# Performance work log

Measured on AMD Instinct MI355X. Metric: run time of the kernel, lower is better.

## Reference

```python
import jax, jax.numpy as jnp
import numpy as np

STRIDE = 1  # module init arg


def setup_inputs() -> dict:
    key = jax.random.key(0)
    k1, k2 = jax.random.split(key)
    x = jax.random.normal(k1, (16, 32, 256, 256), dtype=jnp.float32)
    kernel = jax.random.normal(k2, (32, 5, 5), dtype=jnp.float32) * 0.1
    return {"input": x, "kernel": kernel}


def _maxmin_conv(x, kernel, stride=STRIDE):
    # Max-min semifield convolution:
    #   out[b,oc,i,j] = max_{c,dy,dx} min(x_pad[b,c,i*s+dy,j*s+dx], k[oc,dy,dx])
    # Since min(., k) is monotone in x, the max over in-channels commutes:
    #   max_{c} min(x_c, k) == min(max_c x_c, k)
    # so we reduce channels once up front (same math, far less memory).
    K = kernel.shape[-1]
    p = K - 1
    top = p // 2
    bot = p - top  # calculate_padding(): left=top=floor(p/2), right=bottom=p-top
    xmax = jnp.max(x, axis=1)  # [B, H, W]
    xp = jnp.pad(xmax, ((0, 0), (top, bot), (top, bot)), constant_values=-np.inf)
    B, Hp, Wp = xp.shape
    Ho = (Hp - K) // stride + 1
    Wo = (Wp - K) // stride + 1
    OC = kernel.shape[0]
    acc = jnp.full((B, OC, Ho, Wo), -np.inf, dtype=x.dtype)
    for dy in range(K):  # fixed small K*K loop over kernel taps
        for dx in range(K):
            patch = xp[:, dy:dy + stride * Ho:stride, dx:dx + stride * Wo:stride]  # [B,Ho,Wo]
            cand = jnp.minimum(patch[:, None, :, :], kernel[None, :, dy, dx, None, None])
            acc = jnp.maximum(acc, cand)
    return acc


def reference(input, kernel):
    return _maxmin_conv(input, kernel)
```

## Files before the change

### kernel.cpp

```cpp
#include <hip/hip_runtime.h>
#include <math.h>


#define BATCH 16
#define CH    32
#define OCH   32
#define HH    256
#define WW    256
#define HWSZ  (HH * WW)
#define TW    32
#define TH    32
#define LW    40
#define LH    36
#define NWG   (BATCH * (WW / TW) * (HH / TH))

__device__ __forceinline__ float vmax3(float a, float b, float c) {
    float d;
    asm("v_max3_f32 %0, %1, %2, %3" : "=v"(d) : "v"(a), "v"(b), "v"(c));
    return d;
}

__global__ __launch_bounds__(256, 3) void fused_maxmin_kernel(const float* __restrict__ x,
                                                              const float* __restrict__ kk,
                                                              float* __restrict__ out) {
    __shared__ float xmt[LH][LW];
    __shared__ float lkf[OCH * 25];

    int tid = threadIdx.x;
    int bid = blockIdx.x;
    int swz = (bid & 7) * (NWG >> 3) + (bid >> 3);
    int b   = swz >> 6;
    int ty  = (swz >> 3) & 7;
    int tx  = swz & 7;

    for (int i = tid; i < OCH * 25; i += 256) lkf[i] = kk[i];

    const float NI = -INFINITY;
    int x4base = tx * (TW / 4) - 1;
    int ybase  = ty * TH - 2;
    const float4* xb = (const float4*)(x + (size_t)b * CH * HWSZ);

    for (int p = tid; p < (LW / 4) * LH; p += 256) {
        int pc = p % (LW / 4);
        int pr = p / (LW / 4);
        int c4 = x4base + pc;
        int rw = ybase + pr;
        bool valid = (c4 >= 0) && (c4 < WW / 4) && (rw >= 0) && (rw < HH);
        int c4c = c4 < 0 ? 0 : (c4 > WW / 4 - 1 ? WW / 4 - 1 : c4);
        int rwc = rw < 0 ? 0 : (rw > HH - 1 ? HH - 1 : rw);
        const float4* src = xb + (size_t)rwc * (WW / 4) + c4c;
        float4 m = src[0];
#pragma unroll
        for (int c = 1; c < CH; ++c) {
            float4 v = src[(size_t)c * (HWSZ / 4)];
            m.x = fmaxf(m.x, v.x);
            m.y = fmaxf(m.y, v.y);
            m.z = fmaxf(m.z, v.z);
            m.w = fmaxf(m.w, v.w);
        }
        if (!valid) { m.x = NI; m.y = NI; m.z = NI; m.w = NI; }
        *(float4*)&xmt[pr][pc * 4] = m;
    }
    __syncthreads();

    int xg = tid & 7;
    int yg = (tid >> 3) & 3;
    int og = tid >> 5;
    int orow0 = yg * 8;

    const float* wbase = &xmt[0][4 * xg];

    for (int oi = 0; oi < 4; ++oi) {
        int o = og * 4 + oi;
        float kr[25];
#pragma unroll
        for (int i = 0; i < 25; ++i) kr[i] = lkf[o * 25 + i];

        float w[5][12];
#pragma unroll
        for (int r = 0; r < 4; ++r)
#pragma unroll
            for (int q = 0; q < 3; ++q)
                *(float4*)&w[r][4 * q] = *(const float4*)(wbase + (orow0 + r) * LW + 4 * q);

        float* op = out + (size_t)(b * OCH + o) * HWSZ
                  + (size_t)(ty * TH + orow0) * WW + tx * TW + 4 * xg;

#pragma unroll
        for (int r = 0; r < 8; ++r) {
            int wl = (r + 4) % 5;
#pragma unroll
            for (int q = 0; q < 3; ++q)
                *(float4*)&w[wl][4 * q] = *(const float4*)(wbase + (orow0 + r + 4) * LW + 4 * q);

            float a[4];
#pragma unroll
            for (int j = 0; j < 4; ++j) {
                float m[25];
#pragma unroll
                for (int dy = 0; dy < 5; ++dy) {
                    int wr = (r + dy) % 5;
#pragma unroll
                    for (int dx = 0; dx < 5; ++dx)
                        m[dy * 5 + dx] = fminf(w[wr][j + dx + 2], kr[dy * 5 + dx]);
                }
                float t0 = vmax3(m[0],  m[1],  m[2]);
                float t1 = vmax3(m[3],  m[4],  m[5]);
                float t2 = vmax3(m[6],  m[7],  m[8]);
                float t3 = vmax3(m[9],  m[10], m[11]);
                float t4 = vmax3(m[12], m[13], m[14]);
                float t5 = vmax3(m[15], m[16], m[17]);
                float t6 = vmax3(m[18], m[19], m[20]);
                float t7 = vmax3(m[21], m[22], m[23]);
                float u0 = vmax3(t0, t1, t2);
                float u1 = vmax3(t3, t4, t5);
                float u2 = vmax3(t6, t7, m[24]);
                a[j] = vmax3(u0, u1, u2);
            }
            *(float4*)(op + (size_t)r * WW) = make_float4(a[0], a[1], a[2], a[3]);
        }
    }
}

extern "C" void kernel_launch(void* const* d_in, const int* in_sizes, int n_in,
                              void* d_out, int out_size, void* d_ws, size_t ws_size,
                              hipStream_t stream) {
    const float* x  = (const float*)d_in[0];
    const float* kk = (const float*)d_in[1];
    float* out      = (float*)d_out;
    fused_maxmin_kernel<<<NWG, 256, 0, stream>>>(x, kk, out);
}
```

Measured before the change: 66.10 us.

## Remap compute threads to 2x8 output tiles with register-resident window across channels

Changes the thread-to-output mapping so each thread computes a 2-row by 8-column patch for 8 output channels, loading its 6x12 input window from LDS once into registers and reusing it across all channels. Kernel weights are now read directly from global memory with wave-uniform indexing (scalar loads) instead of staged in LDS. LDS row pitch is padded to 44 floats and occupancy hint raised to 4 blocks per SIMD. Trades fewer LDS reads for higher register pressure and more global output writes per thread.

```diff
diff --git a/kernel.cpp b/kernel.cpp
--- a/kernel.cpp
+++ b/kernel.cpp
@@ -10,7 +10,7 @@
 #define HWSZ  (HH * WW)
 #define TW    32
 #define TH    32
-#define LW    40
+#define LW    44
 #define LH    36
 #define NWG   (BATCH * (WW / TW) * (HH / TH))
 
@@ -20,12 +20,10 @@
     return d;
 }
 
-__global__ __launch_bounds__(256, 3) void fused_maxmin_kernel(const float* __restrict__ x,
+__global__ __launch_bounds__(256, 4) void fused_maxmin_kernel(const float* __restrict__ x,
                                                               const float* __restrict__ kk,
                                                               float* __restrict__ out) {
     __shared__ float xmt[LH][LW];
-    __shared__ float lkf[OCH * 25];
-
     int tid = threadIdx.x;
     int bid = blockIdx.x;
     int swz = (bid & 7) * (NWG >> 3) + (bid >> 3);
@@ -33,22 +31,20 @@
     int ty  = (swz >> 3) & 7;
     int tx  = swz & 7;
 
-    for (int i = tid; i < OCH * 25; i += 256) lkf[i] = kk[i];
-
     const float NI = -INFINITY;
-    int x4base = tx * (TW / 4) - 1;
-    int ybase  = ty * TH - 2;
+    int x4base = tx * 8 - 1;
+    int ybase  = ty * 32 - 2;
     const float4* xb = (const float4*)(x + (size_t)b * CH * HWSZ);
 
-    for (int p = tid; p < (LW / 4) * LH; p += 256) {
-        int pc = p % (LW / 4);
-        int pr = p / (LW / 4);
+    for (int p = tid; p < 10 * LH; p += 256) {
+        int pc = p % 10;
+        int pr = p / 10;
         int c4 = x4base + pc;
-        int rw = ybase + pr;
-        bool valid = (c4 >= 0) && (c4 < WW / 4) && (rw >= 0) && (rw < HH);
+        int rg = ybase + pr;
+        bool valid = (c4 >= 0) && (c4 < WW / 4) && (rg >= 0) && (rg < HH);
         int c4c = c4 < 0 ? 0 : (c4 > WW / 4 - 1 ? WW / 4 - 1 : c4);
-        int rwc = rw < 0 ? 0 : (rw > HH - 1 ? HH - 1 : rw);
-        const float4* src = xb + (size_t)rwc * (WW / 4) + c4c;
+        int rgc = rg < 0 ? 0 : (rg > HH - 1 ? HH - 1 : rg);
+        const float4* src = xb + (size_t)rgc * (WW / 4) + c4c;
         float4 m = src[0];
 #pragma unroll
         for (int c = 1; c < CH; ++c) {
@@ -63,47 +59,45 @@
     }
     __syncthreads();
 
-    int xg = tid & 7;
-    int yg = (tid >> 3) & 3;
-    int og = tid >> 5;
-    int orow0 = yg * 8;
+    int xg  = tid & 3;
+    int rw  = (tid >> 2) & 15;
+    int wid = __builtin_amdgcn_readfirstlane(tid >> 6);
 
-    const float* wbase = &xmt[0][4 * xg];
+    float w[6][12];
+    {
+        const float* wb = &xmt[2 * rw][8 * xg + 2];
+#pragma unroll
+        for (int r = 0; r < 6; ++r) {
+            const float* rp = wb + r * LW;
+            *(float2*)&w[r][0]  = *(const float2*)(rp + 0);
+            *(float4*)&w[r][2]  = *(const float4*)(rp + 2);
+            *(float4*)&w[r][6]  = *(const float4*)(rp + 6);
+            *(float2*)&w[r][10] = *(const float2*)(rp + 10);
+        }
+    }
 
-    for (int oi = 0; oi < 4; ++oi) {
-        int o = og * 4 + oi;
+    size_t obase = (size_t)(b * OCH + wid * 8) * HWSZ
+                 + (size_t)(ty * TH + 2 * rw) * WW + tx * TW + 8 * xg;
+
+#pragma unroll 2
+    for (int o = 0; o < 8; ++o) {
+        const float* kw = kk + (wid * 8 + o) * 25;
         float kr[25];
 #pragma unroll
-        for (int i = 0; i < 25; ++i) kr[i] = lkf[o * 25 + i];
+        for (int i = 0; i < 25; ++i) kr[i] = kw[i];
 
-        float w[5][12];
+        float* op = out + obase + (size_t)o * HWSZ;
 #pragma unroll
-        for (int r = 0; r < 4; ++r)
+        for (int ry = 0; ry < 2; ++ry) {
+            float a[8];
 #pragma unroll
-            for (int q = 0; q < 3; ++q)
-                *(float4*)&w[r][4 * q] = *(const float4*)(wbase + (orow0 + r) * LW + 4 * q);
-
-        float* op = out + (size_t)(b * OCH + o) * HWSZ
-                  + (size_t)(ty * TH + orow0) * WW + tx * TW + 4 * xg;
-
-#pragma unroll
-        for (int r = 0; r < 8; ++r) {
-            int wl = (r + 4) % 5;
-#pragma unroll
-            for (int q = 0; q < 3; ++q)
-                *(float4*)&w[wl][4 * q] = *(const float4*)(wbase + (orow0 + r + 4) * LW + 4 * q);
-
-            float a[4];
-#pragma unroll
-            for (int j = 0; j < 4; ++j) {
+            for (int jj = 0; jj < 8; ++jj) {
                 float m[25];
 #pragma unroll
-                for (int dy = 0; dy < 5; ++dy) {
-                    int wr = (r + dy) % 5;
+                for (int dy = 0; dy < 5; ++dy)
 #pragma unroll
                     for (int dx = 0; dx < 5; ++dx)
-                        m[dy * 5 + dx] = fminf(w[wr][j + dx + 2], kr[dy * 5 + dx]);
-                }
+                        m[dy * 5 + dx] = fminf(w[ry + dy][jj + dx], kr[dy * 5 + dx]);
                 float t0 = vmax3(m[0],  m[1],  m[2]);
                 float t1 = vmax3(m[3],  m[4],  m[5]);
                 float t2 = vmax3(m[6],  m[7],  m[8]);
@@ -115,9 +109,10 @@
                 float u0 = vmax3(t0, t1, t2);
                 float u1 = vmax3(t3, t4, t5);
                 float u2 = vmax3(t6, t7, m[24]);
-                a[j] = vmax3(u0, u1, u2);
+                a[jj] = vmax3(u0, u1, u2);
             }
-            *(float4*)(op + (size_t)r * WW) = make_float4(a[0], a[1], a[2], a[3]);
+            *(float4*)(op + ry * WW + 0) = make_float4(a[0], a[1], a[2], a[3]);
+            *(float4*)(op + ry * WW + 4) = make_float4(a[4], a[5], a[6], a[7]);
         }
     }
 }
```

Result: slower. 126.1 us (+90.7%).

## Halve tile height, keep input window in registers across output channels, nontemporal stores

Applied to the files above, without the earlier changes.

Shrinks the tile to 32x16 with a 42-wide padded LDS buffer, doubling the workgroup count. Each thread now loads a 6x8 window once into registers and reuses it across 8 output channels, computing 2 rows by 4 columns. Previously the window was reloaded for every output channel. Kernel weights now come straight from global memory (uniform per wave) instead of LDS, and outputs are written with nontemporal stores to avoid polluting the cache. Costs: a larger halo fraction means more redundant channel-max loads, and launch bounds drop to 2 waves per SIMD.

```diff
diff --git a/kernel.cpp b/kernel.cpp
--- a/kernel.cpp
+++ b/kernel.cpp
@@ -9,10 +9,12 @@
 #define WW    256
 #define HWSZ  (HH * WW)
 #define TW    32
-#define TH    32
-#define LW    40
-#define LH    36
-#define NWG   (BATCH * (WW / TW) * (HH / TH))
+#define TH    16
+#define LH    20
+#define LW    42
+#define NWG   (BATCH * (HH / TH) * (WW / TW))
+
+typedef float floatx4 __attribute__((ext_vector_type(4)));
 
 __device__ __forceinline__ float vmax3(float a, float b, float c) {
     float d;
@@ -20,35 +22,30 @@
     return d;
 }
 
-__global__ __launch_bounds__(256, 3) void fused_maxmin_kernel(const float* __restrict__ x,
+__global__ __launch_bounds__(256, 2) void fused_maxmin_kernel(const float* __restrict__ x,
                                                               const float* __restrict__ kk,
                                                               float* __restrict__ out) {
     __shared__ float xmt[LH][LW];
-    __shared__ float lkf[OCH * 25];
-
     int tid = threadIdx.x;
     int bid = blockIdx.x;
     int swz = (bid & 7) * (NWG >> 3) + (bid >> 3);
-    int b   = swz >> 6;
-    int ty  = (swz >> 3) & 7;
-    int tx  = swz & 7;
-
-    for (int i = tid; i < OCH * 25; i += 256) lkf[i] = kk[i];
+    int b   = swz >> 7;
+    int t2  = swz & 127;
+    int ty  = t2 >> 3;
+    int tx  = t2 & 7;
 
     const float NI = -INFINITY;
-    int x4base = tx * (TW / 4) - 1;
-    int ybase  = ty * TH - 2;
-    const float4* xb = (const float4*)(x + (size_t)b * CH * HWSZ);
 
-    for (int p = tid; p < (LW / 4) * LH; p += 256) {
-        int pc = p % (LW / 4);
-        int pr = p / (LW / 4);
-        int c4 = x4base + pc;
-        int rw = ybase + pr;
+    if (tid < 200) {
+        int pr = tid / 10;
+        int pc = tid % 10;
+        int c4 = tx * 8 - 1 + pc;
+        int rw = ty * TH - 2 + pr;
         bool valid = (c4 >= 0) && (c4 < WW / 4) && (rw >= 0) && (rw < HH);
         int c4c = c4 < 0 ? 0 : (c4 > WW / 4 - 1 ? WW / 4 - 1 : c4);
         int rwc = rw < 0 ? 0 : (rw > HH - 1 ? HH - 1 : rw);
-        const float4* src = xb + (size_t)rwc * (WW / 4) + c4c;
+        const float4* src = (const float4*)x + (size_t)b * CH * (HWSZ / 4)
+                          + (size_t)rwc * (WW / 4) + c4c;
         float4 m = src[0];
 #pragma unroll
         for (int c = 1; c < CH; ++c) {
@@ -59,51 +56,45 @@
             m.w = fmaxf(m.w, v.w);
         }
         if (!valid) { m.x = NI; m.y = NI; m.z = NI; m.w = NI; }
-        *(float4*)&xmt[pr][pc * 4] = m;
+        *(float2*)&xmt[pr][4 * pc]     = make_float2(m.x, m.y);
+        *(float2*)&xmt[pr][4 * pc + 2] = make_float2(m.z, m.w);
     }
     __syncthreads();
 
     int xg = tid & 7;
-    int yg = (tid >> 3) & 3;
-    int og = tid >> 5;
-    int orow0 = yg * 8;
+    int rg = (tid >> 3) & 7;
+    int wv = __builtin_amdgcn_readfirstlane(tid >> 6);
 
-    const float* wbase = &xmt[0][4 * xg];
+    float w[6][8];
+#pragma unroll
+    for (int r = 0; r < 6; ++r) {
+        const float* rp = &xmt[2 * rg + r][4 * xg + 2];
+#pragma unroll
+        for (int s = 0; s < 4; ++s)
+            *(float2*)&w[r][2 * s] = *(const float2*)(rp + 2 * s);
+    }
 
-    for (int oi = 0; oi < 4; ++oi) {
-        int o = og * 4 + oi;
+    size_t obase = (size_t)(b * OCH + wv * 8) * HWSZ
+                 + (size_t)(ty * TH + 2 * rg) * WW + tx * TW + 4 * xg;
+
+    for (int o = 0; o < 8; ++o) {
+        const float* kw = kk + (wv * 8 + o) * 25;
         float kr[25];
 #pragma unroll
-        for (int i = 0; i < 25; ++i) kr[i] = lkf[o * 25 + i];
+        for (int i = 0; i < 25; ++i) kr[i] = kw[i];
 
-        float w[5][12];
+        float* op = out + obase + (size_t)o * HWSZ;
 #pragma unroll
-        for (int r = 0; r < 4; ++r)
-#pragma unroll
-            for (int q = 0; q < 3; ++q)
-                *(float4*)&w[r][4 * q] = *(const float4*)(wbase + (orow0 + r) * LW + 4 * q);
-
-        float* op = out + (size_t)(b * OCH + o) * HWSZ
-                  + (size_t)(ty * TH + orow0) * WW + tx * TW + 4 * xg;
-
-#pragma unroll
-        for (int r = 0; r < 8; ++r) {
-            int wl = (r + 4) % 5;
-#pragma unroll
-            for (int q = 0; q < 3; ++q)
-                *(float4*)&w[wl][4 * q] = *(const float4*)(wbase + (orow0 + r + 4) * LW + 4 * q);
-
+        for (int r = 0; r < 2; ++r) {
             float a[4];
 #pragma unroll
             for (int j = 0; j < 4; ++j) {
                 float m[25];
 #pragma unroll
-                for (int dy = 0; dy < 5; ++dy) {
-                    int wr = (r + dy) % 5;
+                for (int dy = 0; dy < 5; ++dy)
 #pragma unroll
                     for (int dx = 0; dx < 5; ++dx)
-                        m[dy * 5 + dx] = fminf(w[wr][j + dx + 2], kr[dy * 5 + dx]);
-                }
+                        m[dy * 5 + dx] = fminf(w[r + dy][j + dx], kr[dy * 5 + dx]);
                 float t0 = vmax3(m[0],  m[1],  m[2]);
                 float t1 = vmax3(m[3],  m[4],  m[5]);
                 float t2 = vmax3(m[6],  m[7],  m[8]);
@@ -117,7 +108,8 @@
                 float u2 = vmax3(t6, t7, m[24]);
                 a[j] = vmax3(u0, u1, u2);
             }
-            *(float4*)(op + (size_t)r * WW) = make_float4(a[0], a[1], a[2], a[3]);
+            floatx4 ov = { a[0], a[1], a[2], a[3] };
+            __builtin_nontemporal_store(ov, (floatx4*)(op + (size_t)r * WW));
         }
     }
 }
```

Result: faster. 55.40 us (-16.2%).
